# Performance work log

Hardware: AMD Instinct MI355X
Metric: run time of the kernel (lower is better)

## Reference

```python
import jax, jax.numpy as jnp
from jax import lax
import numpy as np

D_MODEL = 1024
D_STATE = 16
D_CONV = 4
EXPAND = 2
D_INNER = EXPAND * D_MODEL  # 2048
DT_RANK = D_MODEL // 16     # 64
BATCH = 4
SEQ = 1024


def setup_inputs() -> dict:
    key = jax.random.key(0)
    ks = iter(jax.random.split(key, 40))
    def w(shape, s=0.02):
        return (s * jax.random.normal(next(ks), shape)).astype(jnp.float32)
    inp = {"x": jax.random.normal(next(ks), (BATCH, SEQ, D_MODEL), dtype=jnp.float32)}
    # S4D-real style A init: A = -exp(A_log), A_log = log(1..N) per channel
    Alog = jnp.log(jnp.tile(jnp.arange(1, D_STATE + 1, dtype=jnp.float32), (D_INNER, 1)))
    for s in ("f", "b"):
        inp[f"inproj_{s}"] = w((D_MODEL, 2 * D_INNER))
        inp[f"conv_w_{s}"] = w((D_INNER, D_CONV), 0.2)
        inp[f"conv_b_{s}"] = jnp.zeros((D_INNER,), jnp.float32)
        inp[f"xproj_{s}"] = w((D_INNER, DT_RANK + 2 * D_STATE))
        inp[f"dt_w_{s}"] = w((DT_RANK, D_INNER))
        inp[f"dt_b_{s}"] = jnp.full((D_INNER,), -4.0, jnp.float32)  # softplus(-4)~0.018
        inp[f"Alog_{s}"] = Alog
        inp[f"Dp_{s}"] = jnp.ones((D_INNER,), jnp.float32)
        inp[f"outproj_{s}"] = w((D_INNER, D_MODEL))
    inp["gate_w"] = w((2 * D_MODEL, D_MODEL))
    inp["gate_b"] = jnp.zeros((D_MODEL,), jnp.float32)
    inp["proj_w"] = w((D_MODEL, D_MODEL))
    inp["proj_b"] = jnp.zeros((D_MODEL,), jnp.float32)
    return inp


def _mamba(x, inproj, conv_w, conv_b, xproj, dt_w, dt_b, Alog, Dp, outproj):
    B, L, _ = x.shape
    xz = x @ inproj                           # [B,L,2*Di]
    u, z = jnp.split(xz, 2, axis=-1)          # each [B,L,Di]
    # depthwise causal conv1d, width D_CONV
    K = conv_w.shape[1]
    up = jnp.pad(u, ((0, 0), (K - 1, 0), (0, 0)))
    uc = conv_b
    for k in range(K):
        uc = uc + up[:, k:k + L, :] * conv_w[:, k]
    uc = jax.nn.silu(uc)                      # [B,L,Di]
    dbl = uc @ xproj                          # [B,L,dt_rank+2N]
    N = Alog.shape[1]
    dt, Bm, Cm = jnp.split(dbl, [DT_RANK, DT_RANK + N], axis=-1)
    delta = jax.nn.softplus(dt @ dt_w + dt_b) # [B,L,Di]
    A = -jnp.exp(Alog)                        # [Di,N]

    def step(h, inp):
        u_t, d_t, B_t, C_t = inp              # [B,Di],[B,Di],[B,N],[B,N]
        dA = jnp.exp(d_t[..., None] * A)      # [B,Di,N]
        h = dA * h + (d_t * u_t)[..., None] * B_t[:, None, :]
        y_t = jnp.einsum('bdn,bn->bd', h, C_t)
        return h, y_t

    h0 = jnp.zeros((B, uc.shape[-1], N), x.dtype)
    xs = (uc.transpose(1, 0, 2), delta.transpose(1, 0, 2),
          Bm.transpose(1, 0, 2), Cm.transpose(1, 0, 2))
    _, ys = lax.scan(step, h0, xs)            # ys: [L,B,Di]
    y = ys.transpose(1, 0, 2) + uc * Dp
    y = y * jax.nn.silu(z)
    return y @ outproj                        # [B,L,d_model]


def reference(x, inproj_f, conv_w_f, conv_b_f, xproj_f, dt_w_f, dt_b_f, Alog_f, Dp_f, outproj_f,
              inproj_b, conv_w_b, conv_b_b, xproj_b, dt_w_b, dt_b_b, Alog_b, Dp_b, outproj_b,
              gate_w, gate_b, proj_w, proj_b):
    y_f = _mamba(x, inproj_f, conv_w_f, conv_b_f, xproj_f, dt_w_f, dt_b_f, Alog_f, Dp_f, outproj_f)
    xb = jnp.flip(x, axis=1)
    y_b = _mamba(xb, inproj_b, conv_w_b, conv_b_b, xproj_b, dt_w_b, dt_b_b, Alog_b, Dp_b, outproj_b)
    y_b = jnp.flip(y_b, axis=1)
    g = jax.nn.sigmoid(jnp.concatenate([y_f, y_b], axis=-1) @ gate_w + gate_b)
    y = g * y_f + (1.0 - g) * y_b
    return y @ proj_w + proj_b
```

## Files before the change

kernel.cpp:

```cpp
#include <hip/hip_runtime.h>
#include <hip/hip_bf16.h>

#define B_  4
#define L_  1024
#define DM  1024
#define DI  2048
#define NS  16
#define RK  64
#define MT  (B_ * L_)
#define NC  32
#define CH  (L_ / NC)
#define KSX 256
#define NZX 8
#define PSZ (B_ * NC * NS * DI)

typedef unsigned short u16;
typedef __attribute__((ext_vector_type(8))) short  bh8;
typedef __attribute__((ext_vector_type(8))) unsigned short us8;
typedef __attribute__((ext_vector_type(8))) _Float16 h8;
typedef __attribute__((ext_vector_type(4))) float  f4;

__device__ __forceinline__ float bf2f(u16 u) {
  union { unsigned int i; float f; } c; c.i = ((unsigned int)u) << 16; return c.f;
}
__device__ __forceinline__ u16 f2bf(float f) {
  union { float f; unsigned int i; } c; c.f = f;
  unsigned int x = c.i;
  unsigned int r = (x + 0x7fffu + ((x >> 16) & 1u)) >> 16;
  return (u16)r;
}

__device__ __forceinline__ void gl16(const u16* g, u16* l) {
  __builtin_amdgcn_global_load_lds(
      (const __attribute__((address_space(1))) void*)g,
      (__attribute__((address_space(3))) void*)l, 16, 0, 0);
}

__device__ __forceinline__ void pow16(float q1, float* dA) {
  float q2 = q1 * q1;
  float q3 = q2 * q1;
  float q4 = q2 * q2;
  float q8 = q4 * q4;
  dA[0] = q1;       dA[1] = q2;       dA[2] = q3;       dA[3] = q4;
  dA[4] = q4 * q1;  dA[5] = q4 * q2;  dA[6] = q4 * q3;  dA[7] = q8;
  dA[8] = q8 * q1;  dA[9] = q8 * q2;  dA[10] = q8 * q3; dA[11] = q8 * q4;
  dA[12] = q8 * dA[4]; dA[13] = q8 * dA[5]; dA[14] = q8 * dA[6];
  dA[15] = q8 * q8;
}

__global__ void detect_k(const unsigned int* __restrict__ alog,
                         int* __restrict__ flag, int* __restrict__ afl) {
  *flag = (alog[0] != 0u) ? 1 : 0;
  afl[0] = 1; afl[1] = 1;
}

__global__ __launch_bounds__(256)
void cvt_k(const void* __restrict__ src, u16* __restrict__ dst, int n,
           const int* __restrict__ flag) {
  int i = blockIdx.x * 256 + threadIdx.x;
  if (i >= n) return;
  if (*flag) dst[i] = ((const u16*)src)[i];
  else       dst[i] = f2bf(((const float*)src)[i]);
}

__global__ __launch_bounds__(256)
void cvt10_k(const int* __restrict__ flagp,
             const void* s0, u16* d0, int n0, const void* s1, u16* d1, int n1,
             const void* s2, u16* d2, int n2, const void* s3, u16* d3, int n3,
             const void* s4, u16* d4, int n4, const void* s5, u16* d5, int n5,
             const void* s6, u16* d6, int n6, const void* s7, u16* d7, int n7,
             const void* s8, u16* d8, int n8, const void* s9, u16* d9, int n9)
{
  const void* s; u16* d; int n;
  switch (blockIdx.y) {
    case 0: s = s0; d = d0; n = n0; break;  case 1: s = s1; d = d1; n = n1; break;
    case 2: s = s2; d = d2; n = n2; break;  case 3: s = s3; d = d3; n = n3; break;
    case 4: s = s4; d = d4; n = n4; break;  case 5: s = s5; d = d5; n = n5; break;
    case 6: s = s6; d = d6; n = n6; break;  case 7: s = s7; d = d7; n = n7; break;
    case 8: s = s8; d = d8; n = n8; break;  default: s = s9; d = d9; n = n9; break;
  }
  int i = blockIdx.x * 256 + threadIdx.x;
  if (i >= n) return;
  d[i] = *flagp ? ((const u16*)s)[i] : f2bf(((const float*)s)[i]);
}

__global__ __launch_bounds__(256)
void a2_k(const int* __restrict__ flagp, const void* __restrict__ sf,
          const void* __restrict__ sb, _Float16* __restrict__ A2h,
          int* __restrict__ afl)
{
  int i = blockIdx.x * 256 + threadIdx.x;
  int dir = i >> 15;
  const void* src = dir ? sb : sf;
  int j = i & (DI * NS - 1);
  float v = *flagp ? bf2f(((const u16*)src)[j]) : ((const float*)src)[j];
  float a2 = -__expf(v);
  A2h[i] = (_Float16)a2;
  int n = i & 15;
  if (fabsf(a2 + (float)(n + 1)) > 1e-3f * (n + 1)) atomicAnd(&afl[dir], 0);
}

struct TpBatch {
  const void* src[8];
  u16* dst[8];
  int R[8], C[8], tilesX[8];
  int tOff[9];
  int cnt;
};

__global__ __launch_bounds__(256)
void tposeB_k(TpBatch tb, const int* __restrict__ flag) {
  __shared__ u16 tile[32][33];
  int bid = blockIdx.x;
  int i = 0;
  #pragma unroll
  for (int q = 0; q < 7; ++q) if (i + 1 < tb.cnt && bid >= tb.tOff[i + 1]) ++i;
  int local = bid - tb.tOff[i];
  int tX = tb.tilesX[i];
  int c0 = (local % tX) * 32, r0 = (local / tX) * 32;
  int R = tb.R[i], C = tb.C[i];
  const void* src = tb.src[i];
  u16* dst = tb.dst[i];
  int tx = threadIdx.x & 31, ty = threadIdx.x >> 5;
  int isbf = *flag;
  #pragma unroll
  for (int k = 0; k < 4; ++k) {
    int r = r0 + ty + k * 8, c = c0 + tx;
    u16 v = 0;
    if (r < R && c < C)
      v = isbf ? ((const u16*)src)[(size_t)r * C + c]
               : f2bf(((const float*)src)[(size_t)r * C + c]);
    tile[ty + k * 8][tx] = v;
  }
  __syncthreads();
  #pragma unroll
  for (int k = 0; k < 4; ++k) {
    int c = c0 + ty + k * 8, r = r0 + tx;
    if (c < C && r < R)
      dst[(size_t)c * R + r] = tile[tx][ty + k * 8];
  }
}

template<int ACT, int CATM, int OUTF, int BIDIR, int SPLITK, int DUO, int XSW, int ZDIR>
__global__ __launch_bounds__(256)
void gemm2(const u16* __restrict__ A, int lda,
           const u16* __restrict__ Wt,
           const u16* __restrict__ bias,
           void* __restrict__ Cp, int ldc, void* __restrict__ C2,
           int M, int N, int K,
           const u16* __restrict__ yfp, const u16* __restrict__ ybp,
           const int* __restrict__ flagp, const u16* __restrict__ Aalt)
{
  __shared__ __align__(16) u16 As[128][64];
  __shared__ __align__(16) u16 Bs[128][64];

  int bx, by;
  if (XSW) {
    int g = blockIdx.y * gridDim.x + blockIdx.x;
    int xcd = g & 7, j = g >> 3;
    int bxb = gridDim.x >> 3;
    int sh = 31 - __builtin_clz(bxb);
    bx = xcd * bxb + (j & (bxb - 1));
    by = j >> sh;
  } else { bx = blockIdx.x; by = blockIdx.y; }

  int zdir = 0, zslice = 0;
  if (ZDIR && SPLITK) { zdir = blockIdx.z >> 3; zslice = blockIdx.z & (NZX - 1); }
  else if (ZDIR)      { zdir = blockIdx.z; }
  else if (SPLITK)    { zslice = blockIdx.z; }

  const int tid  = threadIdx.x;
  const int lane = tid & 63;
  const int w    = tid >> 6;
  const int wm   = (w >> 1) * 64, wn = (w & 1) * 64;
  const int bm0  = by * 128, bn0 = bx * 128;
  const int l15  = lane & 15, quad = lane >> 4;
  const int rI8  = lane >> 3;
  const int cG8  = (lane & 7) ^ rI8;

  const u16* Wtp = ZDIR ? (Wt + (size_t)zdir * N * K) : Wt;

  f4 acc[4][4] = {};

  const int kb = SPLITK ? zslice * KSX : 0;
  const int ke = SPLITK ? kb + KSX : K;

  for (int k0 = kb; k0 < ke; k0 += 64) {
    {
      const u16* Abase;
      if (ZDIR)     Abase = zdir ? Aalt : A;
      else if (DUO) Abase = (bn0 < DM) ? A : ybp;
      else          Abase = A;
      #pragma unroll
      for (int t = 0; t < 4; ++t) {
        int rb = w * 32 + t * 8;
        int row = rb + rI8;
        const u16* gp;
        if (CATM) {
          int kk = k0 + cG8 * 8;
          int m = bm0 + row;
          gp = (kk < DM) ? (yfp + (size_t)m * DM + kk)
                         : (ybp + (size_t)(m ^ (L_ - 1)) * DM + (kk - DM));
        } else {
          gp = Abase + (size_t)(bm0 + row) * lda + k0 + cG8 * 8;
        }
        gl16(gp, &As[rb][0]);
      }
    }
    #pragma unroll
    for (int t = 0; t < 4; ++t) {
      int rb = w * 32 + t * 8;
      int row = rb + rI8;
      int n = bn0 + row; if (n > N - 1) n = N - 1;
      gl16(Wtp + (size_t)n * K + k0 + cG8 * 8, &Bs[rb][0]);
    }
    __syncthreads();
    #pragma unroll
    for (int s = 0; s < 2; ++s) {
      bh8 af[4], bg[4];
      const int phys = ((quad + 4 * s) ^ (l15 & 7)) * 8;
      #pragma unroll
      for (int i = 0; i < 4; ++i) {
        af[i] = *(const bh8*)&As[wm + i * 16 + l15][phys];
        bg[i] = *(const bh8*)&Bs[wn + i * 16 + l15][phys];
      }
      #pragma unroll
      for (int i = 0; i < 4; ++i)
        #pragma unroll
        for (int j = 0; j < 4; ++j)
          acc[i][j] = __builtin_amdgcn_mfma_f32_16x16x32_bf16(af[i], bg[j], acc[i][j], 0, 0, 0);
    }
    __syncthreads();
  }

  const int obf = (OUTF == 1) ? *flagp : 1;
  #pragma unroll
  for (int j = 0; j < 4; ++j) {
    int lcol = bn0 + wn + j * 16 + l15;
    if (lcol >= N) continue;
    int col = BIDIR ? (lcol & 4095) : (DUO ? (lcol & (DM - 1)) : lcol);
    float bv = bias ? bf2f(bias[(ZDIR ? zdir * N : 0) + col]) : 0.f;
    #pragma unroll
    for (int i = 0; i < 4; ++i) {
      #pragma unroll
      for (int r = 0; r < 4; ++r) {
        int row = bm0 + wm + i * 16 + quad * 4 + r;
        float v = acc[i][j][r] + bv;
        if (ACT == 1) v = (v > 20.f) ? v : __logf(1.f + __expf(v));
        if (ACT == 3) {
          float g = 1.f / (1.f + __expf(-v));
          float fv = bf2f(yfp[(size_t)row * DM + col]);
          float bb = bf2f(ybp[(size_t)(row ^ (L_ - 1)) * DM + col]);
          v = g * fv + (1.f - g) * bb;
        }
        if (BIDIR) {
          u16* base = (lcol < 4096) ? (u16*)Cp : (u16*)C2;
          int orow = (lcol < 4096) ? row : (row ^ (L_ - 1));
          u16* dst = (col < DI) ? (base + (size_t)orow * DI + col)
                                : (base + (size_t)(8u << 20) + (size_t)orow * DI + (col - DI));
          *dst = f2bf(v);
        } else if (DUO) {
          if (lcol < DM) ((u16*)Cp)[(size_t)row * ldc + col] = f2bf(v);
          else           ((u16*)C2)[(size_t)row * ldc + col] = f2bf(v);
        } else if (ZDIR) {
          u16* base = zdir ? (u16*)C2 : (u16*)Cp;
          base[(size_t)row * ldc + col] = f2bf(v);
        } else if (OUTF == 1 && !obf) {
          ((float*)Cp)[(size_t)row * ldc + col] = v;
        } else {
          ((u16*)Cp)[(size_t)row * ldc + col] = f2bf(v);
        }
      }
    }
  }
}


__global__ __launch_bounds__(256)
void gemmxp(const u16* __restrict__ uc,
            const u16* __restrict__ Wt,
            float* __restrict__ xpf, float* __restrict__ xpb)
{
  const int by  = blockIdx.x;
  const int dir = blockIdx.y >> 3, zsl = blockIdx.y & 7;
  const int bm0 = by * 128;
  const int kb  = zsl * KSX;
  const int tid = threadIdx.x, lane = tid & 63, w = tid >> 6;
  const int wm  = (w >> 1) * 64, wn = (w & 1) * 64;
  const int l15 = lane & 15, quad = lane >> 4;
  const u16* Ab = uc + (size_t)dir * MT * DI;
  const u16* Bb = Wt + (size_t)dir * 96 * DI;

  f4 acc[4][4] = {};
  #pragma unroll
  for (int ks = 0; ks < KSX / 32; ++ks) {
    const int ko = kb + ks * 32 + quad * 8;
    bh8 a[4], b[4];
    #pragma unroll
    for (int i = 0; i < 4; ++i)
      a[i] = *(const bh8*)&Ab[(size_t)(bm0 + wm + i * 16 + l15) * DI + ko];
    #pragma unroll
    for (int j = 0; j < 4; ++j) {
      int n = wn + j * 16 + l15; if (n > 95) n = 95;
      b[j] = *(const bh8*)&Bb[(size_t)n * DI + ko];
    }
    #pragma unroll
    for (int i = 0; i < 4; ++i)
      #pragma unroll
      for (int j = 0; j < 4; ++j)
        acc[i][j] = __builtin_amdgcn_mfma_f32_16x16x32_bf16(a[i], b[j], acc[i][j], 0, 0, 0);
  }
  float* P = (dir ? xpb : xpf) + (size_t)zsl * MT * 96;
  #pragma unroll
  for (int j = 0; j < 4; ++j) {
    int col = wn + j * 16 + l15;
    if (col >= 96) continue;
    #pragma unroll
    for (int i = 0; i < 4; ++i)
      #pragma unroll
      for (int r = 0; r < 4; ++r) {
        int row = bm0 + wm + i * 16 + quad * 4 + r;
        P[(size_t)row * 96 + col] = acc[i][j][r];
      }
  }
}

__global__ __launch_bounds__(256)
void gemmdtw(const u16* __restrict__ dbl,
             const u16* __restrict__ Wt,
             const u16* __restrict__ bias,
             u16* __restrict__ Df, u16* __restrict__ Db)
{
  const int dir = blockIdx.z;
  const int bn0 = blockIdx.x * 128;
  const int bm0 = blockIdx.y * 128;
  const int tid = threadIdx.x, lane = tid & 63, w = tid >> 6;
  const int wm  = (w >> 1) * 64, wn = (w & 1) * 64;
  const int l15 = lane & 15, quad = lane >> 4;
  const u16* Ab = dbl + (size_t)dir * MT * 96;
  const u16* Bb = Wt + (size_t)dir * DI * RK;

  f4 acc[4][4] = {};
  #pragma unroll
  for (int s = 0; s < 2; ++s) {
    const int ko = s * 32 + quad * 8;
    bh8 a[4], b[4];
    #pragma unroll
    for (int i = 0; i < 4; ++i)
      a[i] = *(const bh8*)&Ab[(size_t)(bm0 + wm + i * 16 + l15) * 96 + ko];
    #pragma unroll
    for (int j = 0; j < 4; ++j)
      b[j] = *(const bh8*)&Bb[(size_t)(bn0 + wn + j * 16 + l15) * RK + ko];
    #pragma unroll
    for (int i = 0; i < 4; ++i)
      #pragma unroll
      for (int j = 0; j < 4; ++j)
        acc[i][j] = __builtin_amdgcn_mfma_f32_16x16x32_bf16(a[i], b[j], acc[i][j], 0, 0, 0);
  }
  u16* D = dir ? Db : Df;
  #pragma unroll
  for (int j = 0; j < 4; ++j) {
    int col = bn0 + wn + j * 16 + l15;
    float bv = bf2f(bias[dir * DI + col]);
    #pragma unroll
    for (int i = 0; i < 4; ++i)
      #pragma unroll
      for (int r = 0; r < 4; ++r) {
        int row = bm0 + wm + i * 16 + quad * 4 + r;
        float v = acc[i][j][r] + bv;
        v = (v > 20.f) ? v : __logf(1.f + __expf(v));
        D[(size_t)row * DI + col] = f2bf(v);
      }
  }
}

__global__ __launch_bounds__(512)
void gemm256i(const u16* __restrict__ A, int lda,
              const u16* __restrict__ Wt, int ldw,
              u16* __restrict__ Cp, u16* __restrict__ C2, int K)
{
  __shared__ __align__(16) u16 As[2][256][64];
  __shared__ __align__(16) u16 Bs[2][256][64];

  int g  = blockIdx.y * gridDim.x + blockIdx.x;
  int id = (g & 7) * ((gridDim.x * gridDim.y) >> 3) + (g >> 3);
  int bx = id >> 4;
  int by = id & 15;

  const int tid  = threadIdx.x;
  const int lane = tid & 63;
  const int w    = tid >> 6;
  const int wm2  = w >> 2;
  const int wn4  = w & 3;
  const int l15  = lane & 15, quad = lane >> 4;
  const int rI8  = lane >> 3;
  const int cG8  = (lane & 7) ^ rI8;
  const int bm0  = by * 256, bn0 = bx * 256;
  const int NT   = K >> 6;

  const u16* Ag = A  + (size_t)(bm0 + w * 8 + rI8) * lda + cG8 * 8;
  const u16* Bg = Wt + (size_t)(bn0 + w * 8 + rI8) * ldw + cG8 * 8;

  auto STAGE = [&](int kt, int bb) {
    const u16* ap = Ag + kt * 64;
    const u16* bp = Bg + kt * 64;
    #pragma unroll
    for (int i = 0; i < 4; ++i) {
      gl16(ap + (size_t)(i * 64) * lda, &As[bb][i * 64 + w * 8][0]);
      gl16(bp + (size_t)(i * 64) * ldw, &Bs[bb][i * 64 + w * 8][0]);
    }
  };

  f4 acc[8][4] = {};

  const int ph0 = ((quad    ) ^ (l15 & 7)) * 8;
  const int ph1 = ((quad + 4) ^ (l15 & 7)) * 8;

  STAGE(0, 0);
  __syncthreads();

  bh8 aA[4], aB[4], aC[4], aD[4], bg0[4], bg1[4];
  #pragma unroll
  for (int x = 0; x < 4; ++x) {
    aA[x]  = *(const bh8*)&As[0][wm2 * 128 + x * 16 + l15][ph0];
    bg0[x] = *(const bh8*)&Bs[0][wn4 * 64  + x * 16 + l15][ph0];
  }

  #pragma unroll 2
  for (int t = 0; t < NT; ++t) {
    const int p = t & 1, q = p ^ 1;
    const bool pre = (t + 1 < NT);

    if (pre) STAGE(t + 1, q);

    #pragma unroll
    for (int x = 0; x < 4; ++x)
      aB[x] = *(const bh8*)&As[p][wm2 * 128 + 64 + x * 16 + l15][ph0];
    __builtin_amdgcn_s_setprio(1);
    #pragma unroll
    for (int i = 0; i < 4; ++i)
      #pragma unroll
      for (int j = 0; j < 4; ++j)
        acc[i][j] = __builtin_amdgcn_mfma_f32_16x16x32_bf16(aA[i], bg0[j], acc[i][j], 0, 0, 0);
    __builtin_amdgcn_s_setprio(0);

    #pragma unroll
    for (int x = 0; x < 4; ++x) {
      aC[x]  = *(const bh8*)&As[p][wm2 * 128 + x * 16 + l15][ph1];
      bg1[x] = *(const bh8*)&Bs[p][wn4 * 64  + x * 16 + l15][ph1];
    }
    __builtin_amdgcn_s_setprio(1);
    #pragma unroll
    for (int i = 0; i < 4; ++i)
      #pragma unroll
      for (int j = 0; j < 4; ++j)
        acc[4 + i][j] = __builtin_amdgcn_mfma_f32_16x16x32_bf16(aB[i], bg0[j], acc[4 + i][j], 0, 0, 0);
    __builtin_amdgcn_s_setprio(0);

    #pragma unroll
    for (int x = 0; x < 4; ++x)
      aD[x] = *(const bh8*)&As[p][wm2 * 128 + 64 + x * 16 + l15][ph1];
    __builtin_amdgcn_s_setprio(1);
    #pragma unroll
    for (int i = 0; i < 4; ++i)
      #pragma unroll
      for (int j = 0; j < 4; ++j)
        acc[i][j] = __builtin_amdgcn_mfma_f32_16x16x32_bf16(aC[i], bg1[j], acc[i][j], 0, 0, 0);
    __builtin_amdgcn_s_setprio(0);

    __syncthreads();
    if (pre) {
      #pragma unroll
      for (int x = 0; x < 4; ++x) {
        aA[x]  = *(const bh8*)&As[q][wm2 * 128 + x * 16 + l15][ph0];
        bg0[x] = *(const bh8*)&Bs[q][wn4 * 64  + x * 16 + l15][ph0];
      }
    }
    __builtin_amdgcn_s_setprio(1);
    #pragma unroll
    for (int i = 0; i < 4; ++i)
      #pragma unroll
      for (int j = 0; j < 4; ++j)
        acc[4 + i][j] = __builtin_amdgcn_mfma_f32_16x16x32_bf16(aD[i], bg1[j], acc[4 + i][j], 0, 0, 0);
    __builtin_amdgcn_s_setprio(0);
  }

  {
    const int lc0  = bn0 + wn4 * 64;
    const int col0 = lc0 & 4095;
    u16* base = (lc0 < 4096) ? Cp : C2;
    u16* dst0 = (col0 < DI) ? base : (base + (size_t)(8u << 20) - DI);
    const int flip = (lc0 < 4096) ? 0 : (L_ - 1);
    #pragma unroll
    for (int i = 0; i < 8; ++i) {
      #pragma unroll
      for (int r = 0; r < 4; ++r) {
        int row = bm0 + wm2 * 128 + i * 16 + quad * 4 + r;
        u16* rp = dst0 + (size_t)(row ^ flip) * DI + col0;
        #pragma unroll
        for (int j = 0; j < 4; ++j)
          rp[j * 16 + l15] = f2bf(acc[i][j][r]);
      }
    }
  }
}

__global__ __launch_bounds__(256)
void rdbl_k(const float* __restrict__ xpf, const float* __restrict__ xpb,
            u16* __restrict__ dbl)
{
  int i = blockIdx.x * 256 + threadIdx.x;
  int dir = i >= MT * 96;
  int il = dir ? (i - MT * 96) : i;
  const float* P = dir ? xpb : xpf;
  float s = 0.f;
  #pragma unroll
  for (int z = 0; z < NZX; ++z) s += P[(size_t)z * MT * 96 + il];
  dbl[i] = f2bf(s);
}

__global__ __launch_bounds__(256)
void conv8_k(const u16* __restrict__ xzu_f, const u16* __restrict__ xzu_b,
             const u16* __restrict__ cw,
             const u16* __restrict__ cb,
             u16* __restrict__ uc)
{
  int g = blockIdx.x * 256 + threadIdx.x;
  int dir = g >> 18;
  int gl = g & ((1 << 18) - 1);
  int d  = (gl & (DI / 8 - 1)) * 8;
  int t0 = ((gl >> 8) & (L_ / 4 - 1)) * 4;
  int b  = gl >> 16;
  const u16* xzu = dir ? xzu_b : xzu_f;
  const u16* cwp = cw + dir * DI * 4;
  const u16* cbp = cb + dir * DI;
  float w[8][4], bias[8];
  {
    u16 wr[32];
    #pragma unroll
    for (int q = 0; q < 4; ++q)
      *(us8*)&wr[q * 8] = *(const us8*)&cwp[d * 4 + q * 8];
    #pragma unroll
    for (int i = 0; i < 8; ++i)
      #pragma unroll
      for (int k = 0; k < 4; ++k) w[i][k] = bf2f(wr[i * 4 + k]);
    us8 cbv = *(const us8*)&cbp[d];
    #pragma unroll
    for (int i = 0; i < 8; ++i) bias[i] = bf2f(cbv[i]);
  }
  float xv[7][8];
  #pragma unroll
  for (int r = 0; r < 7; ++r) {
    int ts = t0 + r - 3;
    if (ts >= 0) {
      us8 v = *(const us8*)&xzu[(size_t)(b * L_ + ts) * DI + d];
      #pragma unroll
      for (int i = 0; i < 8; ++i) xv[r][i] = bf2f(v[i]);
    } else {
      #pragma unroll
      for (int i = 0; i < 8; ++i) xv[r][i] = 0.f;
    }
  }
  #pragma unroll
  for (int o = 0; o < 4; ++o) {
    us8 out;
    #pragma unroll
    for (int i = 0; i < 8; ++i) {
      float a = bias[i];
      #pragma unroll
      for (int k = 0; k < 4; ++k) a += xv[o + k][i] * w[i][k];
      out[i] = f2bf(a / (1.f + __expf(-a)));
    }
    *(us8*)&uc[(size_t)dir * MT * DI + (size_t)(b * L_ + t0 + o) * DI + d] = out;
  }
}

__global__ __launch_bounds__(256, 4)
void scanA_k(const u16* __restrict__ delta, const u16* __restrict__ uc,
             const u16* __restrict__ dbl, const _Float16* __restrict__ A2h,
             const int* __restrict__ afl,
             _Float16* __restrict__ P, _Float16* __restrict__ S)
{
  int g = blockIdx.x * 256 + threadIdx.x;
  int dir = g >> 18;
  int gl = g & ((1 << 18) - 1);
  int d = gl & (DI - 1);
  int c = (gl >> 11) & (NC - 1);
  int b = gl >> 16;
  delta += (size_t)dir * MT * DI;
  uc    += (size_t)dir * MT * DI;
  dbl   += (size_t)dir * MT * 96;
  P     += (size_t)dir * PSZ;
  S     += (size_t)dir * PSZ;
  const int fast = afl[dir];
  float A2[NS];
  if (!fast) {
    h8 a0 = *(const h8*)&A2h[((size_t)dir * DI + d) * NS];
    h8 a1 = *(const h8*)&A2h[((size_t)dir * DI + d) * NS + 8];
    #pragma unroll
    for (int n = 0; n < 8; ++n) { A2[n] = (float)a0[n]; A2[n + 8] = (float)a1[n]; }
  }
  float Pv[NS], Sv[NS];
  #pragma unroll
  for (int n = 0; n < NS; ++n) { Pv[n] = 1.f; Sv[n] = 0.f; }
  int t0 = c * CH;
  for (int t = t0; t < t0 + CH; ++t) {
    size_t row = (size_t)b * L_ + t;
    float dv = bf2f(delta[row * DI + d]);
    float uv = bf2f(uc[row * DI + d]);
    float du = dv * uv;
    us8 b0 = *(const us8*)&dbl[row * 96 + 64];
    us8 b1 = *(const us8*)&dbl[row * 96 + 72];
    if (fast) {
      float dA[NS];
      pow16(__expf(-dv), dA);
      #pragma unroll
      for (int n = 0; n < NS; ++n) {
        float Bv = (n < 8) ? bf2f(b0[n & 7]) : bf2f(b1[n & 7]);
        Sv[n] = fmaf(dA[n], Sv[n], du * Bv);
        Pv[n] *= dA[n];
      }
    } else {
      #pragma unroll
      for (int n = 0; n < NS; ++n) {
        float Bv = (n < 8) ? bf2f(b0[n & 7]) : bf2f(b1[n & 7]);
        float dA = __expf(dv * A2[n]);
        Sv[n] = fmaf(dA, Sv[n], du * Bv);
        Pv[n] *= dA;
      }
    }
  }
  size_t base = ((size_t)(b * NC + c) * NS) * DI + d;
  #pragma unroll
  for (int n = 0; n < NS; ++n) {
    P[base + (size_t)n * DI] = (_Float16)Pv[n];
    S[base + (size_t)n * DI] = (_Float16)Sv[n];
  }
}

__global__ __launch_bounds__(256)
void scanB_k(_Float16* __restrict__ P, const _Float16* __restrict__ S)
{
  int g = blockIdx.x * 256 + threadIdx.x;
  int dir = g >> 17;
  int gl = g & ((1 << 17) - 1);
  int d = gl & (DI - 1);
  int n = (gl >> 11) & (NS - 1);
  int b = gl >> 15;
  P += (size_t)dir * PSZ;
  S += (size_t)dir * PSZ;
  float h = 0.f;
  #pragma unroll 4
  for (int c = 0; c < NC; ++c) {
    size_t ix = ((size_t)(b * NC + c) * NS + n) * DI + d;
    float p = (float)P[ix], s = (float)S[ix];
    P[ix] = (_Float16)h;
    h = fmaf(p, h, s);
  }
}

__global__ __launch_bounds__(256, 4)
void scanC_k(const u16* __restrict__ uc, const u16* delta,
             const u16* __restrict__ dbl, const u16* __restrict__ xzz_f,
             const u16* __restrict__ xzz_b, const _Float16* __restrict__ A2h,
             const int* __restrict__ afl, const u16* __restrict__ Dp,
             const _Float16* __restrict__ hstart, u16* ys)
{
  int g = blockIdx.x * 256 + threadIdx.x;
  int dir = g >> 18;
  int gl = g & ((1 << 18) - 1);
  int d = gl & (DI - 1);
  int c = (gl >> 11) & (NC - 1);
  int b = gl >> 16;
  const u16* xzz = dir ? xzz_b : xzz_f;
  uc     += (size_t)dir * MT * DI;
  delta  += (size_t)dir * MT * DI;
  dbl    += (size_t)dir * MT * 96;
  Dp     += dir * DI;
  hstart += (size_t)dir * PSZ;
  ys     += (size_t)dir * MT * DI;
  const int fast = afl[dir];
  float A2[NS], h[NS];
  if (!fast) {
    h8 a0 = *(const h8*)&A2h[((size_t)dir * DI + d) * NS];
    h8 a1 = *(const h8*)&A2h[((size_t)dir * DI + d) * NS + 8];
    #pragma unroll
    for (int n = 0; n < 8; ++n) { A2[n] = (float)a0[n]; A2[n + 8] = (float)a1[n]; }
  }
  float Dv = bf2f(Dp[d]);
  size_t hbase = ((size_t)(b * NC + c) * NS) * DI + d;
  #pragma unroll
  for (int n = 0; n < NS; ++n) h[n] = (float)hstart[hbase + (size_t)n * DI];
  int t0 = c * CH;
  for (int t = t0; t < t0 + CH; ++t) {
    size_t row = (size_t)b * L_ + t;
    float dv = bf2f(delta[row * DI + d]);
    float uv = bf2f(uc[row * DI + d]);
    float du = dv * uv;
    us8 b0 = *(const us8*)&dbl[row * 96 + 64];
    us8 b1 = *(const us8*)&dbl[row * 96 + 72];
    us8 c0 = *(const us8*)&dbl[row * 96 + 80];
    us8 c1 = *(const us8*)&dbl[row * 96 + 88];
    float y;
    if (fast) {
      float dA[NS];
      pow16(__expf(-dv), dA);
      float y0 = 0.f, y1 = 0.f, y2 = 0.f, y3 = 0.f;
      #pragma unroll
      for (int n = 0; n < NS; ++n) {
        float Bv = (n < 8) ? bf2f(b0[n & 7]) : bf2f(b1[n & 7]);
        float Cv = (n < 8) ? bf2f(c0[n & 7]) : bf2f(c1[n & 7]);
        h[n] = fmaf(dA[n], h[n], du * Bv);
        float hv = h[n] * Cv;
        if ((n & 3) == 0) y0 += hv;
        else if ((n & 3) == 1) y1 += hv;
        else if ((n & 3) == 2) y2 += hv;
        else y3 += hv;
      }
      y = (y0 + y1) + (y2 + y3);
    } else {
      float y0 = 0.f, y1 = 0.f, y2 = 0.f, y3 = 0.f;
      #pragma unroll
      for (int n = 0; n < NS; ++n) {
        float Bv = (n < 8) ? bf2f(b0[n & 7]) : bf2f(b1[n & 7]);
        float Cv = (n < 8) ? bf2f(c0[n & 7]) : bf2f(c1[n & 7]);
        float dA = __expf(dv * A2[n]);
        h[n] = fmaf(dA, h[n], du * Bv);
        float hv = h[n] * Cv;
        if ((n & 3) == 0) y0 += hv;
        else if ((n & 3) == 1) y1 += hv;
        else if ((n & 3) == 2) y2 += hv;
        else y3 += hv;
      }
      y = (y0 + y1) + (y2 + y3);
    }
    float z = bf2f(xzz[row * DI + d]);
    float out = (y + uv * Dv) * (z / (1.f + __expf(-z)));
    ys[row * DI + d] = f2bf(out);
  }
}

extern "C" void kernel_launch(void* const* d_in, const int* in_sizes, int n_in,
                              void* d_out, int out_size, void* d_ws, size_t ws_size,
                              hipStream_t stream)
{
  char* ws = (char*)d_ws;
  const size_t MB = 1ull << 20;
  const size_t KB = 1024;

  u16* xzu_f   = (u16*)(ws + 0);
  u16* xzz_f   = (u16*)(ws + 16 * MB);
  u16* xzu_b   = (u16*)(ws + 32 * MB);
  u16* xzz_b   = (u16*)(ws + 48 * MB);
  u16* uc      = (u16*)(ws + 64 * MB);
  u16* delta_f = (u16*)(ws + 96 * MB);
  u16* delta_b = (u16*)(ws + 112 * MB);
  u16* dbl     = (u16*)(ws + 128 * MB);
  char* SM     = ws + 128 * MB + 1536 * KB;
  u16* w_convw = (u16*)(SM);
  u16* w_convb = (u16*)(SM + 32 * KB);
  u16* w_dtb   = (u16*)(SM + 40 * KB);
  u16* w_dp    = (u16*)(SM + 48 * KB);
  u16* w_gb    = (u16*)(SM + 56 * KB);
  u16* w_pb    = (u16*)(SM + 58 * KB);
  int* flag    = (int*)(SM + 60 * KB);
  int* afl     = (int*)(SM + 60 * KB + 8);
  _Float16* A2h = (_Float16*)(ws + 128 * MB + 1600 * KB);
  u16* xproj_t2 = (u16*)(ws + 128 * MB + 1728 * KB);
  u16* dtw_t2   = (u16*)(ws + 128 * MB + 2496 * KB);
  u16* xc       = uc;
  u16* inproj_t = delta_f;
  float* xpart_f = (float*)delta_f;
  float* xpart_b = (float*)delta_b;
  _Float16* Pb   = (_Float16*)xzu_f;
  _Float16* Sb   = (_Float16*)xzu_b;
  u16* outp2_t  = (u16*)(ws + 80 * MB);
  u16* gw_t     = (u16*)(ws + 88 * MB);
  u16* pw_t     = (u16*)(ws + 92 * MB);
  u16* yf       = xzz_f;
  u16* yb       = xzz_b;
  u16* yc       = (u16*)(ws + 0);

  dim3 blk(256);
  detect_k<<<1, 1, 0, stream>>>((const unsigned int*)d_in[7], flag, afl);

  cvt10_k<<<dim3(32, 10), blk, 0, stream>>>(flag,
      d_in[2],  w_convw,            DI * 4, d_in[3],  w_convb,      DI,
      d_in[6],  w_dtb,              DI,     d_in[8],  w_dp,         DI,
      d_in[11], w_convw + DI * 4,   DI * 4, d_in[12], w_convb + DI, DI,
      d_in[15], w_dtb + DI,         DI,     d_in[17], w_dp + DI,    DI,
      d_in[20], w_gb,               DM,     d_in[22], w_pb,         DM);
  a2_k<<<2 * DI * NS / 256, blk, 0, stream>>>(flag, d_in[7], d_in[16], A2h, afl);
  cvt_k<<<MT * DM / 256, blk, 0, stream>>>(d_in[0], xc, MT * DM, flag);

  {
    TpBatch tb{};
    auto add = [&](int i, const void* s, u16* d, int R, int C) {
      tb.src[i] = s; tb.dst[i] = d; tb.R[i] = R; tb.C[i] = C;
      tb.tilesX[i] = (C + 31) / 32;
      tb.tOff[i + 1] = tb.tOff[i] + tb.tilesX[i] * ((R + 31) / 32);
    };
    tb.tOff[0] = 0;
    add(0, d_in[1],  inproj_t,               DM, 2 * DI);
    add(1, d_in[10], inproj_t + 4096 * 1024, DM, 2 * DI);
    add(2, d_in[4],  xproj_t2,               DI, 96);
    add(3, d_in[13], xproj_t2 + 96 * 2048,   DI, 96);
    add(4, d_in[5],  dtw_t2,                 RK, DI);
    add(5, d_in[14], dtw_t2 + 2048 * 64,     RK, DI);
    tb.cnt = 6;
    tposeB_k<<<tb.tOff[6], blk, 0, stream>>>(tb, flag);
  }

  gemm256i<<<dim3(32, 16), dim3(512), 0, stream>>>(
      xc, DM, inproj_t, DM, xzu_f, xzu_b, DM);

  conv8_k<<<2 * MT * DI / 32 / 256, blk, 0, stream>>>(
      xzu_f, xzu_b, w_convw, w_convb, uc);

  gemmxp<<<dim3(32, 2 * NZX), blk, 0, stream>>>(uc, xproj_t2, xpart_f, xpart_b);
  rdbl_k<<<2 * MT * 96 / 256, blk, 0, stream>>>(xpart_f, xpart_b, dbl);

  gemmdtw<<<dim3(16, 32, 2), blk, 0, stream>>>(dbl, dtw_t2, w_dtb,
                                               delta_f, delta_b);

  scanA_k<<<2 * B_ * NC * DI / 256, blk, 0, stream>>>(
      delta_f, uc, dbl, A2h, afl, Pb, Sb);
  scanB_k<<<2 * B_ * NS * DI / 256, blk, 0, stream>>>(Pb, Sb);
  scanC_k<<<2 * B_ * NC * DI / 256, blk, 0, stream>>>(
      uc, delta_f, dbl, xzz_f, xzz_b, A2h, afl, w_dp, Pb, delta_f);

  {
    TpBatch tb{};
    auto add = [&](int i, const void* s, u16* d, int R, int C) {
      tb.src[i] = s; tb.dst[i] = d; tb.R[i] = R; tb.C[i] = C;
      tb.tilesX[i] = (C + 31) / 32;
      tb.tOff[i + 1] = tb.tOff[i] + tb.tilesX[i] * ((R + 31) / 32);
    };
    tb.tOff[0] = 0;
    add(0, d_in[9],  outp2_t,               DI, DM);
    add(1, d_in[18], outp2_t + 1024 * 2048, DI, DM);
    add(2, d_in[19], gw_t,                  2 * DM, DM);
    add(3, d_in[21], pw_t,                  DM, DM);
    tb.cnt = 4;
    tposeB_k<<<tb.tOff[4], blk, 0, stream>>>(tb, flag);
  }

  gemm2<0, 0, 0, 0, 0, 1, 1, 0><<<dim3(16, 32), blk, 0, stream>>>(
      delta_f, DI, outp2_t, nullptr, yf, DM, yb, MT, 2 * DM, DI,
      nullptr, delta_b, flag, nullptr);

  gemm2<3, 1, 0, 0, 0, 0, 1, 0><<<dim3(8, 32), blk, 0, stream>>>(
      yf, DM, gw_t, w_gb, yc, DM, nullptr, MT, DM, 2 * DM, yf, yb, flag, nullptr);
  gemm2<0, 0, 1, 0, 0, 0, 1, 0><<<dim3(8, 32), blk, 0, stream>>>(
      yc, DM, pw_t, w_pb, d_out, DM, nullptr, MT, DM, DM,
      nullptr, nullptr, flag, nullptr);
}
```

Before: 601.8 us.

## Replace output GEMMs with triple-buffered 512-thread pipelined MFMA kernel

```diff
diff --git a/kernel.cpp b/kernel.cpp
--- a/kernel.cpp
+++ b/kernel.cpp
@@ -141,130 +141,136 @@
   }
 }
 
-template<int ACT, int CATM, int OUTF, int BIDIR, int SPLITK, int DUO, int XSW, int ZDIR>
-__global__ __launch_bounds__(256)
-void gemm2(const u16* __restrict__ A, int lda,
+template<int ACT, int CATM, int OUTF, int DUO>
+__global__ __launch_bounds__(512)
+void gemm3(const u16* __restrict__ A, int lda,
            const u16* __restrict__ Wt,
            const u16* __restrict__ bias,
            void* __restrict__ Cp, int ldc, void* __restrict__ C2,
            int M, int N, int K,
            const u16* __restrict__ yfp, const u16* __restrict__ ybp,
-           const int* __restrict__ flagp, const u16* __restrict__ Aalt)
-{
-  __shared__ __align__(16) u16 As[128][64];
-  __shared__ __align__(16) u16 Bs[128][64];
-
-  int bx, by;
-  if (XSW) {
-    int g = blockIdx.y * gridDim.x + blockIdx.x;
-    int xcd = g & 7, j = g >> 3;
-    int bxb = gridDim.x >> 3;
-    int sh = 31 - __builtin_clz(bxb);
-    bx = xcd * bxb + (j & (bxb - 1));
-    by = j >> sh;
-  } else { bx = blockIdx.x; by = blockIdx.y; }
-
-  int zdir = 0, zslice = 0;
-  if (ZDIR && SPLITK) { zdir = blockIdx.z >> 3; zslice = blockIdx.z & (NZX - 1); }
-  else if (ZDIR)      { zdir = blockIdx.z; }
-  else if (SPLITK)    { zslice = blockIdx.z; }
+           const int* __restrict__ flagp)
+{
+  __shared__ __align__(16) u16 As[3][128][64];
+  __shared__ __align__(16) u16 Bs[3][128][64];
+
+  int g   = blockIdx.y * gridDim.x + blockIdx.x;
+  int xcd = g & 7, jj = g >> 3;
+  int bxb = gridDim.x >> 3;
+  int sh  = 31 - __builtin_clz(bxb);
+  int bx  = xcd * bxb + (jj & (bxb - 1));
+  int by  = jj >> sh;
 
   const int tid  = threadIdx.x;
   const int lane = tid & 63;
   const int w    = tid >> 6;
-  const int wm   = (w >> 1) * 64, wn = (w & 1) * 64;
+  const int wm   = (w >> 2) * 64;
+  const int wn   = (w & 3) * 32;
   const int bm0  = by * 128, bn0 = bx * 128;
   const int l15  = lane & 15, quad = lane >> 4;
   const int rI8  = lane >> 3;
   const int cG8  = (lane & 7) ^ rI8;
-
-  const u16* Wtp = ZDIR ? (Wt + (size_t)zdir * N * K) : Wt;
-
-  f4 acc[4][4] = {};
-
-  const int kb = SPLITK ? zslice * KSX : 0;
-  const int ke = SPLITK ? kb + KSX : K;
-
-  for (int k0 = kb; k0 < ke; k0 += 64) {
-    {
-      const u16* Abase;
-      if (ZDIR)     Abase = zdir ? Aalt : A;
-      else if (DUO) Abase = (bn0 < DM) ? A : ybp;
-      else          Abase = A;
-      #pragma unroll
-      for (int t = 0; t < 4; ++t) {
-        int rb = w * 32 + t * 8;
-        int row = rb + rI8;
-        const u16* gp;
-        if (CATM) {
-          int kk = k0 + cG8 * 8;
-          int m = bm0 + row;
-          gp = (kk < DM) ? (yfp + (size_t)m * DM + kk)
-                         : (ybp + (size_t)(m ^ (L_ - 1)) * DM + (kk - DM));
-        } else {
-          gp = Abase + (size_t)(bm0 + row) * lda + k0 + cG8 * 8;
-        }
-        gl16(gp, &As[rb][0]);
-      }
-    }
-    #pragma unroll
-    for (int t = 0; t < 4; ++t) {
-      int rb = w * 32 + t * 8;
+  const int NT   = K >> 6;
+
+  auto STAGE = [&](int kt, int bb) {
+    const int k0 = kt * 64;
+    #pragma unroll
+    for (int t = 0; t < 2; ++t) {
+      int rb = w * 16 + t * 8;
       int row = rb + rI8;
+      const u16* gp;
+      if (CATM) {
+        int kk = k0 + cG8 * 8;
+        int m = bm0 + row;
+        gp = (kk < DM) ? (yfp + (size_t)m * DM + kk)
+                       : (ybp + (size_t)(m ^ (L_ - 1)) * DM + (kk - DM));
+      } else if (DUO) {
+        const u16* Ab = (bn0 < DM) ? A : ybp;
+        gp = Ab + (size_t)(bm0 + row) * lda + k0 + cG8 * 8;
+      } else {
+        gp = A + (size_t)(bm0 + row) * lda + k0 + cG8 * 8;
+      }
+      gl16(gp, &As[bb][rb][0]);
       int n = bn0 + row; if (n > N - 1) n = N - 1;
-      gl16(Wtp + (size_t)n * K + k0 + cG8 * 8, &Bs[rb][0]);
-    }
-    __syncthreads();
-    #pragma unroll
-    for (int s = 0; s < 2; ++s) {
-      bh8 af[4], bg[4];
-      const int phys = ((quad + 4 * s) ^ (l15 & 7)) * 8;
-      #pragma unroll
-      for (int i = 0; i < 4; ++i) {
-        af[i] = *(const bh8*)&As[wm + i * 16 + l15][phys];
-        bg[i] = *(const bh8*)&Bs[wn + i * 16 + l15][phys];
-      }
-      #pragma unroll
-      for (int i = 0; i < 4; ++i)
-        #pragma unroll
-        for (int j = 0; j < 4; ++j)
-          acc[i][j] = __builtin_amdgcn_mfma_f32_16x16x32_bf16(af[i], bg[j], acc[i][j], 0, 0, 0);
-    }
-    __syncthreads();
+      gl16(Wt + (size_t)n * K + k0 + cG8 * 8, &Bs[bb][rb][0]);
+    }
+  };
+
+  f4 acc[4][2] = {};
+  const int ph0 = ((quad    ) ^ (l15 & 7)) * 8;
+  const int ph1 = ((quad + 4) ^ (l15 & 7)) * 8;
+
+  STAGE(0, 0);
+  STAGE(1, 1);
+  asm volatile("s_waitcnt vmcnt(4)" ::: "memory");
+  __builtin_amdgcn_s_barrier();
+
+  bh8 aA[4], bg0[2], aC[4], bg1[2];
+  #pragma unroll
+  for (int x = 0; x < 4; ++x) aA[x] = *(const bh8*)&As[0][wm + x * 16 + l15][ph0];
+  #pragma unroll
+  for (int x = 0; x < 2; ++x) bg0[x] = *(const bh8*)&Bs[0][wn + x * 16 + l15][ph0];
+
+  int cur = 0, nx1 = 1, nx2 = 2;
+  for (int t = 0; t < NT; ++t) {
+    const bool pre2 = (t + 2 < NT), pre1 = (t + 1 < NT);
+
+    if (pre2) STAGE(t + 2, nx2);
+
+    #pragma unroll
+    for (int x = 0; x < 4; ++x) aC[x] = *(const bh8*)&As[cur][wm + x * 16 + l15][ph1];
+    #pragma unroll
+    for (int x = 0; x < 2; ++x) bg1[x] = *(const bh8*)&Bs[cur][wn + x * 16 + l15][ph1];
+    __builtin_amdgcn_s_setprio(1);
+    #pragma unroll
+    for (int i = 0; i < 4; ++i)
+      #pragma unroll
+      for (int j = 0; j < 2; ++j)
+        acc[i][j] = __builtin_amdgcn_mfma_f32_16x16x32_bf16(aA[i], bg0[j], acc[i][j], 0, 0, 0);
+    __builtin_amdgcn_s_setprio(0);
+
+    if (pre2) { asm volatile("s_waitcnt vmcnt(4) lgkmcnt(0)" ::: "memory"); }
+    else      { asm volatile("s_waitcnt vmcnt(0) lgkmcnt(0)" ::: "memory"); }
+    __builtin_amdgcn_s_barrier();
+    if (pre1) {
+      #pragma unroll
+      for (int x = 0; x < 4; ++x) aA[x] = *(const bh8*)&As[nx1][wm + x * 16 + l15][ph0];
+      #pragma unroll
+      for (int x = 0; x < 2; ++x) bg0[x] = *(const bh8*)&Bs[nx1][wn + x * 16 + l15][ph0];
+    }
+    __builtin_amdgcn_s_setprio(1);
+    #pragma unroll
+    for (int i = 0; i < 4; ++i)
+      #pragma unroll
+      for (int j = 0; j < 2; ++j)
+        acc[i][j] = __builtin_amdgcn_mfma_f32_16x16x32_bf16(aC[i], bg1[j], acc[i][j], 0, 0, 0);
+    __builtin_amdgcn_s_setprio(0);
+
+    int tmp = cur; cur = nx1; nx1 = nx2; nx2 = tmp;
   }
 
   const int obf = (OUTF == 1) ? *flagp : 1;
   #pragma unroll
-  for (int j = 0; j < 4; ++j) {
+  for (int j = 0; j < 2; ++j) {
     int lcol = bn0 + wn + j * 16 + l15;
     if (lcol >= N) continue;
-    int col = BIDIR ? (lcol & 4095) : (DUO ? (lcol & (DM - 1)) : lcol);
-    float bv = bias ? bf2f(bias[(ZDIR ? zdir * N : 0) + col]) : 0.f;
+    int col = DUO ? (lcol & (DM - 1)) : lcol;
+    float bv = bias ? bf2f(bias[col]) : 0.f;
     #pragma unroll
     for (int i = 0; i < 4; ++i) {
       #pragma unroll
       for (int r = 0; r < 4; ++r) {
         int row = bm0 + wm + i * 16 + quad * 4 + r;
         float v = acc[i][j][r] + bv;
-        if (ACT == 1) v = (v > 20.f) ? v : __logf(1.f + __expf(v));
         if (ACT == 3) {
-          float g = 1.f / (1.f + __expf(-v));
+          float gg = 1.f / (1.f + __expf(-v));
           float fv = bf2f(yfp[(size_t)row * DM + col]);
           float bb = bf2f(ybp[(size_t)(row ^ (L_ - 1)) * DM + col]);
-          v = g * fv + (1.f - g) * bb;
+          v = gg * fv + (1.f - gg) * bb;
         }
-        if (BIDIR) {
-          u16* base = (lcol < 4096) ? (u16*)Cp : (u16*)C2;
-          int orow = (lcol < 4096) ? row : (row ^ (L_ - 1));
-          u16* dst = (col < DI) ? (base + (size_t)orow * DI + col)
-                                : (base + (size_t)(8u << 20) + (size_t)orow * DI + (col - DI));
-          *dst = f2bf(v);
-        } else if (DUO) {
+        if (DUO) {
           if (lcol < DM) ((u16*)Cp)[(size_t)row * ldc + col] = f2bf(v);
           else           ((u16*)C2)[(size_t)row * ldc + col] = f2bf(v);
-        } else if (ZDIR) {
-          u16* base = zdir ? (u16*)C2 : (u16*)Cp;
-          base[(size_t)row * ldc + col] = f2bf(v);
         } else if (OUTF == 1 && !obf) {
           ((float*)Cp)[(size_t)row * ldc + col] = v;
         } else {
@@ -845,13 +851,14 @@
     tposeB_k<<<tb.tOff[4], blk, 0, stream>>>(tb, flag);
   }
 
-  gemm2<0, 0, 0, 0, 0, 1, 1, 0><<<dim3(16, 32), blk, 0, stream>>>(
+  gemm3<0, 0, 0, 1><<<dim3(16, 32), dim3(512), 0, stream>>>(
       delta_f, DI, outp2_t, nullptr, yf, DM, yb, MT, 2 * DM, DI,
-      nullptr, delta_b, flag, nullptr);
-
-  gemm2<3, 1, 0, 0, 0, 0, 1, 0><<<dim3(8, 32), blk, 0, stream>>>(
-      yf, DM, gw_t, w_gb, yc, DM, nullptr, MT, DM, 2 * DM, yf, yb, flag, nullptr);
-  gemm2<0, 0, 1, 0, 0, 0, 1, 0><<<dim3(8, 32), blk, 0, stream>>>(
+      nullptr, delta_b, flag);
+
+  gemm3<3, 1, 0, 0><<<dim3(8, 32), dim3(512), 0, stream>>>(
+      yf, DM, gw_t, w_gb, yc, DM, nullptr, MT, DM, 2 * DM, yf, yb, flag);
+
+  gemm3<0, 0, 1, 0><<<dim3(8, 32), dim3(512), 0, stream>>>(
       yc, DM, pw_t, w_pb, d_out, DM, nullptr, MT, DM, DM,
-      nullptr, nullptr, flag, nullptr);
-}
+      nullptr, nullptr, flag);
+}
```

New measurement: 568.4 us. 5.6% less time.
